# Optimization experiments

Measured on AMD Instinct MI355X. Metric: run time of the kernel, lower is better.

Reference implementation:

```python
import jax, jax.numpy as jnp
import numpy as np

N_ATOMS = 200_000
N_PAIRS = 8_000_000
N_CH = 4
EXPONENT = 1.0  # p in 1/r^p potential


def setup_inputs() -> dict:
    key = jax.random.key(0)
    k1, k2, k3 = jax.random.split(key, 3)
    charges = jax.random.normal(k1, (N_ATOMS, N_CH), dtype=jnp.float32)
    neighbor_indices = jax.random.randint(k2, (N_PAIRS, 2), 0, N_ATOMS, dtype=jnp.int32)
    # distances within a physical cutoff shell, bounded away from 0 to keep 1/r^p finite
    neighbor_distances = jax.random.uniform(k3, (N_PAIRS,), dtype=jnp.float32, minval=0.5, maxval=5.0)
    return {
        "charges": charges,
        "neighbor_indices": neighbor_indices,
        "neighbor_distances": neighbor_distances,
    }


def reference(charges, neighbor_indices, neighbor_distances):
    # non-periodic path: potentials_bare = InversePowerLawPotential.from_dist(r) = 1/r^p
    potentials_bare = neighbor_distances ** (-EXPONENT)  # [n_pairs]
    atom_is = neighbor_indices[:, 0]
    atom_js = neighbor_indices[:, 1]
    w = potentials_bare[:, None]  # [n_pairs, 1]
    contributions_is = charges[atom_js] * w  # gather j-charges, scale by pair potential
    contributions_js = charges[atom_is] * w  # gather i-charges (half neighbor list symmetrization)
    potential = jnp.zeros_like(charges)
    potential = potential.at[atom_is].add(contributions_is)
    potential = potential.at[atom_js].add(contributions_js)  # use_half_neighborlist=True
    return potential / 2
```

## Files before the change

kernel.cpp:

```cpp
#include <hip/hip_runtime.h>
#include <hip/hip_fp16.h>


#define BLOCK 1024
#define NSLICES 10
#define CT_BLOCK 256
#define SC_BLOCK 256
#define SC_PPT 8
#define SC_NENT (SC_BLOCK * SC_PPT * 2)
#define CA_BITS 12
#define NCHUNK 49
#define NSLOT (NCHUNK * 4)
#define PLANE_PAD 16
#define CAP_MIN 345024u
#define FB_NSL 10
#define FB_UNROLL 8

__device__ __forceinline__ void fadd(float* p, float v) {
#if defined(__HIP_DEVICE_COMPILE__)
    unsafeAtomicAdd(p, v);
#else
    atomicAdd(p, v);
#endif
}

__device__ __forceinline__ void pkadd(__half2* p, float lo, float hi) {
#if defined(__HIP_DEVICE_COMPILE__)
    __half2 v = __float22half2_rn(make_float2(lo, hi));
    unsigned bits;
    __builtin_memcpy(&bits, &v, 4);
    unsigned off = (unsigned)(unsigned long long)(void*)p;
    asm volatile("ds_pk_add_f16 %0, %1" :: "v"(off), "v"(bits) : "memory");
#else
    (void)p; (void)lo; (void)hi;
#endif
}

__device__ __forceinline__ void lds_drain() {
#if defined(__HIP_DEVICE_COMPILE__)
    asm volatile("s_waitcnt lgkmcnt(0)" ::: "memory");
#endif
}

__global__ void cursor_init(unsigned* __restrict__ cursors, unsigned cap)
{
    int b = threadIdx.x;
    if (b < NCHUNK) cursors[b] = (unsigned)b * cap;
}

__global__ __launch_bounds__(CT_BLOCK) void bucket_count(
    const int4* __restrict__ idx2, unsigned* __restrict__ counts, int npairs)
{
    __shared__ unsigned ph[CT_BLOCK * NCHUNK];
    unsigned* mine = ph + threadIdx.x * NCHUNK;
#pragma unroll
    for (int b = 0; b < NCHUNK; ++b) mine[b] = 0;
    __syncthreads();

    const int n4 = npairs >> 1;
    const int stride = gridDim.x * CT_BLOCK;
    for (int q = blockIdx.x * CT_BLOCK + threadIdx.x; q < n4; q += stride) {
        int4 v = idx2[q];
        ++mine[(unsigned)v.x >> CA_BITS];
        ++mine[(unsigned)v.y >> CA_BITS];
        ++mine[(unsigned)v.z >> CA_BITS];
        ++mine[(unsigned)v.w >> CA_BITS];
    }
    if ((npairs & 1) && blockIdx.x == 0 && threadIdx.x == 0) {
        const int2* idx = (const int2*)idx2;
        int2 ij = idx[npairs - 1];
        ++mine[(unsigned)ij.x >> CA_BITS];
        ++mine[(unsigned)ij.y >> CA_BITS];
    }
    __syncthreads();

    for (int b = threadIdx.x; b < NCHUNK; b += CT_BLOCK) {
        unsigned s = 0;
#pragma unroll 8
        for (int t = 0; t < CT_BLOCK; ++t) s += ph[t * NCHUNK + b];
        if (s) atomicAdd(&counts[b], s);
    }
}

__global__ void bucket_prefix(const unsigned* __restrict__ counts,
                              unsigned* __restrict__ offsets,
                              unsigned* __restrict__ cursors, int nbuckets)
{
    if (threadIdx.x == 0 && blockIdx.x == 0) {
        unsigned acc = 0;
        for (int b = 0; b < nbuckets; ++b) {
            offsets[b] = acc; cursors[b] = acc; acc += counts[b];
        }
        offsets[nbuckets] = acc;
    }
}

template<bool FIX>
__global__ __launch_bounds__(SC_BLOCK) void bucket_scatter(
    const int2*  __restrict__ idx, const float* __restrict__ dist,
    uint2* __restrict__ entries, unsigned* __restrict__ cursors, int npairs,
    unsigned cap)
{
    __shared__ unsigned hist[NSLOT];
    __shared__ unsigned lbase[NSLOT];
    __shared__ unsigned rbase[NSLOT];
    __shared__ unsigned scanbuf[SC_BLOCK];
    __shared__ uint2    stage[SC_NENT];
    __shared__ unsigned char slotid[SC_NENT];
    for (int b = threadIdx.x; b < NSLOT; b += SC_BLOCK) hist[b] = 0;
    __syncthreads();

    const int p0 = blockIdx.x * (SC_BLOCK * SC_PPT) + threadIdx.x;
    const unsigned r = threadIdx.x & 3;
    unsigned key[2 * SC_PPT];
    unsigned brk[2 * SC_PPT];
    float    wv[SC_PPT];

#pragma unroll
    for (int k = 0; k < SC_PPT; ++k) {
        int p = p0 + k * SC_BLOCK;
        if (p < npairs) {
            int2 ij = idx[p];
            wv[k] = 0.5f / dist[p];
            unsigned s0 = (((unsigned)ij.x >> CA_BITS) << 2) + r;
            unsigned s1 = (((unsigned)ij.y >> CA_BITS) << 2) + r;
            key[2 * k]     = (unsigned)ij.y | (((unsigned)ij.x & ((1u << CA_BITS) - 1)) << 18);
            brk[2 * k]     = s0 | (atomicAdd(&hist[s0], 1u) << 8);
            key[2 * k + 1] = (unsigned)ij.x | (((unsigned)ij.y & ((1u << CA_BITS) - 1)) << 18);
            brk[2 * k + 1] = s1 | (atomicAdd(&hist[s1], 1u) << 8);
        } else {
            brk[2 * k] = brk[2 * k + 1] = 0xFFFFFFFFu;
        }
    }
    __syncthreads();

    {
        const int t = threadIdx.x;
        unsigned v = (t < NSLOT) ? hist[t] : 0u;
        scanbuf[t] = v;
        __syncthreads();
        for (int off = 1; off < SC_BLOCK; off <<= 1) {
            unsigned x = (t >= off) ? scanbuf[t - off] : 0u;
            __syncthreads();
            scanbuf[t] += x;
            __syncthreads();
        }
        if (t < NSLOT) lbase[t] = scanbuf[t] - v;
    }
    if (threadIdx.x < NCHUNK) {
        int b = threadIdx.x;
        unsigned h0 = hist[4 * b], h1 = hist[4 * b + 1], h2 = hist[4 * b + 2], h3 = hist[4 * b + 3];
        unsigned tot = h0 + h1 + h2 + h3;
        unsigned g = tot ? atomicAdd(&cursors[b], tot) : 0u;
        if (FIX && tot) {
            unsigned lim = (unsigned)(b + 1) * cap;
            if (g + tot > lim) g = lim - tot;
        }
        rbase[4 * b]     = g;
        rbase[4 * b + 1] = g + h0;
        rbase[4 * b + 2] = g + h0 + h1;
        rbase[4 * b + 3] = g + h0 + h1 + h2;
    }
    __syncthreads();

#pragma unroll
    for (int k = 0; k < SC_PPT; ++k) {
        if (brk[2 * k] != 0xFFFFFFFFu) {
            unsigned wb = __float_as_uint(wv[k]);
            unsigned s0 = brk[2 * k] & 255u,     rk0 = brk[2 * k] >> 8;
            unsigned s1 = brk[2 * k + 1] & 255u, rk1 = brk[2 * k + 1] >> 8;
            unsigned l0 = lbase[s0] + rk0;
            unsigned l1 = lbase[s1] + rk1;
            stage[l0] = make_uint2(key[2 * k], wb);
            slotid[l0] = (unsigned char)s0;
            stage[l1] = make_uint2(key[2 * k + 1], wb);
            slotid[l1] = (unsigned char)s1;
        }
    }
    __syncthreads();

    const unsigned total = scanbuf[NSLOT - 1];
    for (unsigned l = threadIdx.x; l < total; l += SC_BLOCK) {
        unsigned s = slotid[l];
        entries[rbase[s] + (l - lbase[s])] = stage[l];
    }
}

template<int CHUNK_ATOMS, bool FIX>
__global__ __launch_bounds__(BLOCK) void bucket_scan(
    const float4* __restrict__ charges, const uint2* __restrict__ entries,
    const unsigned* obc, uint2* __restrict__ slabs,
    int natoms, unsigned cap)
{
    constexpr int PLANE = CHUNK_ATOMS + PLANE_PAD;
    extern __shared__ __half2 sm2[];
    __half2* smp0 = sm2;
    __half2* smp1 = sm2 + PLANE;

    const int c  = blockIdx.x / NSLICES;
    const int s  = blockIdx.x - c * NSLICES;
    {
        unsigned* z = (unsigned*)sm2;
        for (int e = threadIdx.x; e < 2 * PLANE; e += BLOCK) z[e] = 0u;
    }
    __syncthreads();

    unsigned beg, cnt;
    if (FIX) {
        beg = (unsigned)c * cap;
        unsigned cur = atomicAdd((unsigned*)obc + c, 0u);
        cnt = min(cur - beg, cap);
    } else {
        beg = obc[c];
        cnt = obc[c + 1] - beg;
    }
    const unsigned e0  = beg + (unsigned)((unsigned long long)cnt * s       / NSLICES);
    const unsigned e1  = beg + (unsigned)((unsigned long long)cnt * (s + 1) / NSLICES);

    auto process = [&](uint2 en) {
        float4 cq = charges[en.x & 0x3FFFFu];
        float w = __uint_as_float(en.y);
        unsigned d = en.x >> 18;
        pkadd(smp0 + d, cq.x * w, cq.y * w);
        pkadd(smp1 + d, cq.z * w, cq.w * w);
    };

    const unsigned e0a = min(e1, (e0 + 1u) & ~1u);
    for (unsigned e = e0 + threadIdx.x; e < e0a; e += BLOCK) process(entries[e]);

    const uint4* ent4 = (const uint4*)entries;
    const unsigned base = e0a >> 1;
    const unsigned n4   = (e1 - e0a) >> 1;
    const unsigned nb   = n4 / (BLOCK * 4);

    unsigned q = base + threadIdx.x;
    for (unsigned b = 0; b < nb; ++b, q += BLOCK * 4) {
        uint4 E[4];
#pragma unroll
        for (int u = 0; u < 4; ++u) E[u] = ent4[q + u * BLOCK];
        float4 cq[8];
#pragma unroll
        for (int u = 0; u < 4; ++u) {
            cq[2 * u]     = charges[E[u].x & 0x3FFFFu];
            cq[2 * u + 1] = charges[E[u].z & 0x3FFFFu];
        }
#pragma unroll
        for (int u = 0; u < 4; ++u) {
            float w0 = __uint_as_float(E[u].y);
            unsigned d0 = E[u].x >> 18;
            pkadd(smp0 + d0, cq[2 * u].x * w0, cq[2 * u].y * w0);
            pkadd(smp1 + d0, cq[2 * u].z * w0, cq[2 * u].w * w0);
            float w1 = __uint_as_float(E[u].w);
            unsigned d1 = E[u].z >> 18;
            pkadd(smp0 + d1, cq[2 * u + 1].x * w1, cq[2 * u + 1].y * w1);
            pkadd(smp1 + d1, cq[2 * u + 1].z * w1, cq[2 * u + 1].w * w1);
        }
    }
    for (unsigned q2 = base + nb * (BLOCK * 4) + threadIdx.x; q2 < base + n4; q2 += BLOCK) {
        uint4 E = ent4[q2];
        process(make_uint2(E.x, E.y));
        process(make_uint2(E.z, E.w));
    }
    for (unsigned e = e0a + 2 * n4 + threadIdx.x; e < e1; e += BLOCK) process(entries[e]);

    lds_drain();
    __syncthreads();

    const int c0 = c * CHUNK_ATOMS;
    const int cn = min(CHUNK_ATOMS, natoms - c0);
    uint2* dst = slabs + (size_t)blockIdx.x * CHUNK_ATOMS;
    for (int a = threadIdx.x; a < cn; a += BLOCK) {
        unsigned b0, b1;
        __builtin_memcpy(&b0, &smp0[a], 4);
        __builtin_memcpy(&b1, &smp1[a], 4);
        dst[a] = make_uint2(b0, b1);
    }
}

template<int CH_ATOMS, int NS>
__global__ __launch_bounds__(256) void chunk_reduce_h(
    const uint2* __restrict__ ws, float4* __restrict__ out, int natoms_total)
{
    int g = blockIdx.x * blockDim.x + threadIdx.x;
    if (g >= natoms_total) return;
    int c = g / CH_ATOMS;
    int local = g - c * CH_ATOMS;
    const uint2* p = ws + ((size_t)c * NS) * CH_ATOMS + local;
    float4 acc = make_float4(0.f, 0.f, 0.f, 0.f);
#pragma unroll
    for (int s = 0; s < NS; ++s) {
        uint2 v = p[(size_t)s * CH_ATOMS];
        __half2 h01, h23;
        __builtin_memcpy(&h01, &v.x, 4);
        __builtin_memcpy(&h23, &v.y, 4);
        float2 f01 = __half22float2(h01);
        float2 f23 = __half22float2(h23);
        acc.x += f01.x; acc.y += f01.y; acc.z += f23.x; acc.w += f23.y;
    }
    out[g] = acc;
}

template<int CH_ELEMS, int NS>
__global__ __launch_bounds__(256) void chunk_reduce(
    const float4* __restrict__ ws, float4* __restrict__ out, int total4)
{
    int g = blockIdx.x * blockDim.x + threadIdx.x;
    if (g >= total4) return;
    constexpr int CH4 = CH_ELEMS / 4;
    int c = g / CH4;
    int local = g - c * CH4;
    const float4* p = ws + ((size_t)c * NS) * CH4 + local;
    float4 acc = make_float4(0.f, 0.f, 0.f, 0.f);
#pragma unroll
    for (int s = 0; s < NS; ++s) {
        float4 v = p[(size_t)s * CH4];
        acc.x += v.x; acc.y += v.y; acc.z += v.z; acc.w += v.w;
    }
    out[g] = acc;
}

template<int CHUNK_ATOMS, bool USE_WS>
__global__ __launch_bounds__(BLOCK) void chunk_scan(
    const float4* __restrict__ charges, const int2* __restrict__ idx,
    const float* __restrict__ dist, float* __restrict__ dest,
    int npairs, int natoms)
{
    constexpr int CH_ELEMS = CHUNK_ATOMS * 4;
    extern __shared__ float sm[];
    const int c  = blockIdx.x / FB_NSL;
    const int s  = blockIdx.x - c * FB_NSL;
    const int c0 = c * CHUNK_ATOMS;
    const int cn = min(CHUNK_ATOMS, natoms - c0);
    for (int e = threadIdx.x; e < CH_ELEMS; e += BLOCK) sm[e] = 0.f;
    __syncthreads();
    const int p0 = (int)((long long)npairs * s       / FB_NSL);
    const int p1 = (int)((long long)npairs * (s + 1) / FB_NSL);
    const int nbatch = (p1 - p0) / (BLOCK * FB_UNROLL);
    int p = p0 + threadIdx.x;
    for (int b = 0; b < nbatch; ++b, p += BLOCK * FB_UNROLL) {
        int2 ij[FB_UNROLL]; float dd[FB_UNROLL];
#pragma unroll
        for (int u = 0; u < FB_UNROLL; ++u) { ij[u] = idx[p + u * BLOCK]; dd[u] = dist[p + u * BLOCK]; }
#pragma unroll
        for (int u = 0; u < FB_UNROLL; ++u) {
            unsigned li = (unsigned)(ij[u].x - c0), lj = (unsigned)(ij[u].y - c0);
            float w = 0.5f / dd[u];
            if (li < (unsigned)cn) {
                float4 cq = charges[ij[u].y]; float* bp = sm + li * 4;
                fadd(bp + 0, cq.x * w); fadd(bp + 1, cq.y * w);
                fadd(bp + 2, cq.z * w); fadd(bp + 3, cq.w * w);
            }
            if (lj < (unsigned)cn) {
                float4 cq = charges[ij[u].x]; float* bp = sm + lj * 4;
                fadd(bp + 0, cq.x * w); fadd(bp + 1, cq.y * w);
                fadd(bp + 2, cq.z * w); fadd(bp + 3, cq.w * w);
            }
        }
    }
    for (; p < p1; p += BLOCK) {
        int2 ij = idx[p];
        unsigned li = (unsigned)(ij.x - c0), lj = (unsigned)(ij.y - c0);
        if (li < (unsigned)cn || lj < (unsigned)cn) {
            float w = 0.5f / dist[p];
            if (li < (unsigned)cn) {
                float4 cq = charges[ij.y]; float* bp = sm + li * 4;
                fadd(bp + 0, cq.x * w); fadd(bp + 1, cq.y * w);
                fadd(bp + 2, cq.z * w); fadd(bp + 3, cq.w * w);
            }
            if (lj < (unsigned)cn) {
                float4 cq = charges[ij.x]; float* bp = sm + lj * 4;
                fadd(bp + 0, cq.x * w); fadd(bp + 1, cq.y * w);
                fadd(bp + 2, cq.z * w); fadd(bp + 3, cq.w * w);
            }
        }
    }
    __syncthreads();
    const int nvalid = cn * 4;
    if (USE_WS) {
        float* dst = dest + (size_t)blockIdx.x * CH_ELEMS;
        for (int e = threadIdx.x; e < nvalid; e += BLOCK) dst[e] = sm[e];
    } else {
        float* dst = dest + (size_t)c0 * 4;
        for (int e = threadIdx.x; e < nvalid; e += BLOCK) fadd(dst + e, sm[e]);
    }
}

extern "C" void kernel_launch(void* const* d_in, const int* in_sizes, int n_in,
                              void* d_out, int out_size, void* d_ws, size_t ws_size,
                              hipStream_t stream) {
    const float4* charges = (const float4*)d_in[0];
    const int2*   idx     = (const int2*)  d_in[1];
    const float*  dist    = (const float*) d_in[2];
    float*        out     = (float*)d_out;

    const int natoms = in_sizes[0] / 4;
    const int npairs = in_sizes[2];
    const int total  = out_size;

    int dev = 0;
    hipGetDevice(&dev);
    int maxShm = 0;
    hipDeviceGetAttribute(&maxShm, hipDeviceAttributeMaxSharedMemoryPerBlock, dev);
    const bool big = (maxShm >= 65536);

    constexpr int CA = 4096, CE = CA * 4;
    const int C    = (natoms + CA - 1) / CA;
    const int grid = C * NSLICES;
    const size_t scan_shm = (size_t)2 * (CA + PLANE_PAD) * sizeof(__half2);

    const size_t ENT_OFF     = 1024;
    const size_t slabh_bytes = (size_t)grid * CA * sizeof(uint2);
    const int sc_grid = (npairs + SC_BLOCK * SC_PPT - 1) / (SC_BLOCK * SC_PPT);
    const bool shape_ok = big && natoms <= (1 << 18) && C == NCHUNK
                          && (total & 3) == 0 && total == 4 * natoms;

    unsigned capb = 0;
    if (ws_size > ENT_OFF + slabh_bytes + 256) {
        size_t cmax = (ws_size - ENT_OFF - slabh_bytes - 256) / ((size_t)NCHUNK * sizeof(uint2));
        capb = (unsigned)((cmax > 480000) ? 480000 : cmax);
        capb &= ~63u;
    }
    const bool fix_ok = shape_ok && capb >= CAP_MIN;

    const size_t ent_bytes_old = (size_t)2 * npairs * sizeof(uint2);
    const size_t slab_off_old  = (ENT_OFF + ent_bytes_old + 255) & ~(size_t)255;
    const bool old_ok = shape_ok && ws_size >= slab_off_old + slabh_bytes;

    if (fix_ok) {
        unsigned* cursors = (unsigned*)((char*)d_ws + 512);
        uint2*    entries = (uint2*)((char*)d_ws + ENT_OFF);
        const size_t slab_off = (ENT_OFF + (size_t)NCHUNK * capb * sizeof(uint2) + 255) & ~(size_t)255;
        uint2*    slabs   = (uint2*)((char*)d_ws + slab_off);

        cursor_init<<<1, 64, 0, stream>>>(cursors, capb);
        bucket_scatter<true><<<sc_grid, SC_BLOCK, 0, stream>>>(
            idx, dist, entries, cursors, npairs, capb);
        hipFuncSetAttribute((const void*)bucket_scan<CA, true>,
                            hipFuncAttributeMaxDynamicSharedMemorySize, (int)scan_shm);
        bucket_scan<CA, true><<<grid, BLOCK, scan_shm, stream>>>(
            charges, entries, cursors, slabs, natoms, capb);
        chunk_reduce_h<CA, NSLICES><<<(natoms + 255) / 256, 256, 0, stream>>>(
            slabs, (float4*)out, natoms);
    } else if (old_ok) {
        unsigned* counts  = (unsigned*)d_ws;
        unsigned* offsets = (unsigned*)((char*)d_ws + 256);
        unsigned* cursors = (unsigned*)((char*)d_ws + 512);
        uint2*    entries = (uint2*)((char*)d_ws + ENT_OFF);
        uint2*    slabs   = (uint2*)((char*)d_ws + slab_off_old);

        hipMemsetAsync(d_ws, 0, 1024, stream);
        bucket_count<<<1024, CT_BLOCK, 0, stream>>>((const int4*)idx, counts, npairs);
        bucket_prefix<<<1, 32, 0, stream>>>(counts, offsets, cursors, C);
        bucket_scatter<false><<<sc_grid, SC_BLOCK, 0, stream>>>(
            idx, dist, entries, cursors, npairs, 0u);
        hipFuncSetAttribute((const void*)bucket_scan<CA, false>,
                            hipFuncAttributeMaxDynamicSharedMemorySize, (int)scan_shm);
        bucket_scan<CA, false><<<grid, BLOCK, scan_shm, stream>>>(
            charges, entries, offsets, slabs, natoms, 0u);
        chunk_reduce_h<CA, NSLICES><<<(natoms + 255) / 256, 256, 0, stream>>>(
            slabs, (float4*)out, natoms);
    } else if (big) {
        const size_t ws_need = (size_t)grid * CE * sizeof(float);
        if (ws_size >= ws_need && (total & 3) == 0) {
            hipFuncSetAttribute((const void*)chunk_scan<CA, true>,
                                hipFuncAttributeMaxDynamicSharedMemorySize, CE * 4);
            chunk_scan<CA, true><<<grid, BLOCK, CE * 4, stream>>>(
                charges, idx, dist, (float*)d_ws, npairs, natoms);
            chunk_reduce<CE, FB_NSL><<<(total / 4 + 255) / 256, 256, 0, stream>>>(
                (const float4*)d_ws, (float4*)out, total / 4);
        } else {
            hipMemsetAsync(d_out, 0, (size_t)total * sizeof(float), stream);
            hipFuncSetAttribute((const void*)chunk_scan<CA, false>,
                                hipFuncAttributeMaxDynamicSharedMemorySize, CE * 4);
            chunk_scan<CA, false><<<grid, BLOCK, CE * 4, stream>>>(
                charges, idx, dist, out, npairs, natoms);
        }
    } else {
        constexpr int CA2 = 2048, CE2 = CA2 * 4;
        const int C2 = (natoms + CA2 - 1) / CA2;
        const int grid2 = C2 * FB_NSL;
        const size_t ws_need = (size_t)grid2 * CE2 * sizeof(float);
        if (ws_size >= ws_need && (total & 3) == 0) {
            chunk_scan<CA2, true><<<grid2, BLOCK, CE2 * 4, stream>>>(
                charges, idx, dist, (float*)d_ws, npairs, natoms);
            chunk_reduce<CE2, FB_NSL><<<(total / 4 + 255) / 256, 256, 0, stream>>>(
                (const float4*)d_ws, (float4*)out, total / 4);
        } else {
            hipMemsetAsync(d_out, 0, (size_t)total * sizeof(float), stream);
            chunk_scan<CA2, false><<<grid2, BLOCK, CE2 * 4, stream>>>(
                charges, idx, dist, out, npairs, natoms);
        }
    }
}
```

Measured before the change: 372.9 us.

## Fuse slice reduction into bucket_scan via last-block-done counter, memset cursors

The separate chunk_reduce_h launch is removed from the main path. Each bucket_scan block now bumps a per-chunk done counter, and the last of the NSLICES blocks sums the fp16 slabs into the float4 output. Cursor initialisation switches from a kernel to hipMemsetAsync, using relative cursors offset by b*cap. This saves one or two kernel launches and the gaps between them. In exchange, a threadfence and atomic are added per block, and the tail reduction for each chunk runs in a single block.

```diff
diff --git a/kernel.cpp b/kernel.cpp
--- a/kernel.cpp
+++ b/kernel.cpp
@@ -42,12 +42,6 @@
 #endif
 }
 
-__global__ void cursor_init(unsigned* __restrict__ cursors, unsigned cap)
-{
-    int b = threadIdx.x;
-    if (b < NCHUNK) cursors[b] = (unsigned)b * cap;
-}
-
 __global__ __launch_bounds__(CT_BLOCK) void bucket_count(
     const int4* __restrict__ idx2, unsigned* __restrict__ counts, int npairs)
 {
@@ -151,10 +145,13 @@
         int b = threadIdx.x;
         unsigned h0 = hist[4 * b], h1 = hist[4 * b + 1], h2 = hist[4 * b + 2], h3 = hist[4 * b + 3];
         unsigned tot = h0 + h1 + h2 + h3;
-        unsigned g = tot ? atomicAdd(&cursors[b], tot) : 0u;
-        if (FIX && tot) {
-            unsigned lim = (unsigned)(b + 1) * cap;
-            if (g + tot > lim) g = lim - tot;
+        unsigned g;
+        if (FIX) {
+            unsigned grel = tot ? atomicAdd(&cursors[b], tot) : 0u;
+            if (tot && grel + tot > cap) grel = cap - tot;
+            g = (unsigned)b * cap + grel;
+        } else {
+            g = tot ? atomicAdd(&cursors[b], tot) : 0u;
         }
         rbase[4 * b]     = g;
         rbase[4 * b + 1] = g + h0;
@@ -190,12 +187,13 @@
 __global__ __launch_bounds__(BLOCK) void bucket_scan(
     const float4* __restrict__ charges, const uint2* __restrict__ entries,
     const unsigned* obc, uint2* __restrict__ slabs,
-    int natoms, unsigned cap)
+    int natoms, unsigned cap, unsigned* done, float4* out4)
 {
     constexpr int PLANE = CHUNK_ATOMS + PLANE_PAD;
     extern __shared__ __half2 sm2[];
     __half2* smp0 = sm2;
     __half2* smp1 = sm2 + PLANE;
+    __shared__ unsigned tick;
 
     const int c  = blockIdx.x / NSLICES;
     const int s  = blockIdx.x - c * NSLICES;
@@ -208,8 +206,8 @@
     unsigned beg, cnt;
     if (FIX) {
         beg = (unsigned)c * cap;
-        unsigned cur = atomicAdd((unsigned*)obc + c, 0u);
-        cnt = min(cur - beg, cap);
+        unsigned fill = atomicAdd((unsigned*)obc + c, 0u);
+        cnt = min(fill, cap);
     } else {
         beg = obc[c];
         cnt = obc[c + 1] - beg;
@@ -274,6 +272,31 @@
         __builtin_memcpy(&b0, &smp0[a], 4);
         __builtin_memcpy(&b1, &smp1[a], 4);
         dst[a] = make_uint2(b0, b1);
+    }
+
+    if constexpr (FIX) {
+        __threadfence();
+        if (threadIdx.x == 0) tick = atomicAdd(&done[c], 1u);
+        __syncthreads();
+        if (tick == NSLICES - 1) {
+            __threadfence();
+            const uint2* src = slabs + (size_t)c * NSLICES * CHUNK_ATOMS;
+            float4* o = out4 + (size_t)c * CHUNK_ATOMS;
+            for (int a = threadIdx.x; a < cn; a += BLOCK) {
+                float4 acc = make_float4(0.f, 0.f, 0.f, 0.f);
+#pragma unroll
+                for (int s2 = 0; s2 < NSLICES; ++s2) {
+                    uint2 v = src[(size_t)s2 * CHUNK_ATOMS + a];
+                    __half2 h01, h23;
+                    __builtin_memcpy(&h01, &v.x, 4);
+                    __builtin_memcpy(&h23, &v.y, 4);
+                    float2 f01 = __half22float2(h01);
+                    float2 f23 = __half22float2(h23);
+                    acc.x += f01.x; acc.y += f01.y; acc.z += f23.x; acc.w += f23.y;
+                }
+                o[a] = acc;
+            }
+        }
     }
 }
 
@@ -428,19 +451,18 @@
 
     if (fix_ok) {
         unsigned* cursors = (unsigned*)((char*)d_ws + 512);
+        unsigned* done    = (unsigned*)((char*)d_ws + 768);
         uint2*    entries = (uint2*)((char*)d_ws + ENT_OFF);
         const size_t slab_off = (ENT_OFF + (size_t)NCHUNK * capb * sizeof(uint2) + 255) & ~(size_t)255;
         uint2*    slabs   = (uint2*)((char*)d_ws + slab_off);
 
-        cursor_init<<<1, 64, 0, stream>>>(cursors, capb);
+        hipMemsetAsync(d_ws, 0, 1024, stream);
         bucket_scatter<true><<<sc_grid, SC_BLOCK, 0, stream>>>(
             idx, dist, entries, cursors, npairs, capb);
         hipFuncSetAttribute((const void*)bucket_scan<CA, true>,
                             hipFuncAttributeMaxDynamicSharedMemorySize, (int)scan_shm);
         bucket_scan<CA, true><<<grid, BLOCK, scan_shm, stream>>>(
-            charges, entries, cursors, slabs, natoms, capb);
-        chunk_reduce_h<CA, NSLICES><<<(natoms + 255) / 256, 256, 0, stream>>>(
-            slabs, (float4*)out, natoms);
+            charges, entries, cursors, slabs, natoms, capb, done, (float4*)out);
     } else if (old_ok) {
         unsigned* counts  = (unsigned*)d_ws;
         unsigned* offsets = (unsigned*)((char*)d_ws + 256);
@@ -456,7 +478,7 @@
         hipFuncSetAttribute((const void*)bucket_scan<CA, false>,
                             hipFuncAttributeMaxDynamicSharedMemorySize, (int)scan_shm);
         bucket_scan<CA, false><<<grid, BLOCK, scan_shm, stream>>>(
-            charges, entries, offsets, slabs, natoms, 0u);
+            charges, entries, offsets, slabs, natoms, 0u, nullptr, nullptr);
         chunk_reduce_h<CA, NSLICES><<<(natoms + 255) / 256, 256, 0, stream>>>(
             slabs, (float4*)out, natoms);
     } else if (big) {
```

After: 616.0 us. 1.65x slower.
